# Performance work log

Hardware: AMD Instinct MI355X
Metric: run time of the kernel (lower is better)

Reference implementation:

```python
import jax, jax.numpy as jnp
import numpy as np

EPS = 1e-5

def _lc(x, w, b, stride, pad):
    # x: [B,H,W]; w: [Ho,Wo,kh,kw]; b: [Ho,Wo]
    Ho, Wo, kh, kw = w.shape
    patches = jax.lax.conv_general_dilated_patches(
        x[:, None], (kh, kw), (stride, stride), [(pad, pad), (pad, pad)])
    # patches: [B, kh*kw, Ho, Wo]
    out = jnp.einsum('bkij,ijk->bij', patches, w.reshape(Ho, Wo, kh * kw))
    return out + b

def _ln2d(x, g, b):
    # torch LayerNorm over the last two (spatial) dims
    mu = x.mean(axis=(1, 2), keepdims=True)
    var = ((x - mu) ** 2).mean(axis=(1, 2), keepdims=True)
    return (x - mu) * jax.lax.rsqrt(var + EPS) * g + b

def _pool(x):
    # MaxPool2d(kernel=2, stride=2) over spatial dims of [B,H,W]
    return jax.lax.reduce_window(x, -jnp.inf, jax.lax.max, (1, 2, 2), (1, 2, 2), 'VALID')

def setup_inputs() -> dict:
    key = jax.random.key(0)
    ks = jax.random.split(key, 32)
    d = {}
    d['x'] = jax.random.normal(ks[0], (64, 128, 128), jnp.float32)
    sizes = [(128, 7), (64, 5), (64, 5), (32, 3), (32, 3), (16, 3)]
    for i, (s, k) in enumerate(sizes, start=1):
        d[f'w{i}'] = jax.random.normal(ks[4 * i], (s, s, k, k), jnp.float32) / k
        d[f'b{i}'] = jax.random.normal(ks[4 * i + 1], (s, s), jnp.float32)
        d[f'g{i}'] = jnp.ones((s, s), jnp.float32)
        d[f'be{i}'] = jnp.zeros((s, s), jnp.float32)
    d['fcw'] = jax.random.normal(ks[30], (1024, 256), jnp.float32) / np.sqrt(256.0)
    d['fcb'] = jax.random.normal(ks[31], (1024,), jnp.float32) * 0.01
    return d

def reference(x, w1, b1, g1, be1, w2, b2, g2, be2, w3, b3, g3, be3,
              w4, b4, g4, be4, w5, b5, g5, be5, w6, b6, g6, be6, fcw, fcb):
    # dropout is identity (eval / p=0)
    h = _pool(_ln2d(jax.nn.relu(_lc(x, w1, b1, 1, 3)), g1, be1))   # [B,64,64]
    h = _ln2d(jax.nn.relu(_lc(h, w2, b2, 1, 2)), g2, be2)          # [B,64,64]
    h = _pool(_ln2d(jax.nn.relu(_lc(h, w3, b3, 1, 2)), g3, be3))   # [B,32,32]
    h = _ln2d(jax.nn.relu(_lc(h, w4, b4, 1, 1)), g4, be4)          # [B,32,32]
    h = _pool(_ln2d(jax.nn.relu(_lc(h, w5, b5, 1, 1)), g5, be5))   # [B,16,16]
    h = _ln2d(jax.nn.relu(_lc(h, w6, b6, 1, 1)), g6, be6)          # [B,16,16]
    h = h.reshape(h.shape[0], -1) @ fcw.T + fcb                    # [B,1024]
    return jax.nn.softmax(h, axis=-1)
```

## Files before the change

kernel.cpp:

```cpp
#include <hip/hip_runtime.h>

#define LN_EPS 1e-5f

constexpr int T1_OFF   = 0;
constexpr int WT2_OFF  = 1048576;
constexpr int WT3_OFF  = WT2_OFF + 102400;
constexpr int WT4_OFF  = WT3_OFF + 102400;
constexpr int WT5_OFF  = WT4_OFF + 9216;
constexpr int WT6_OFF  = WT5_OFF + 9216;
constexpr int FCWT_OFF = WT6_OFF + 2304;

constexpr int NREP = 136;

__global__ __launch_bounds__(256) void s1_conv(const float* __restrict__ x,
                                               const float* __restrict__ w1,
                                               const float* __restrict__ b1,
                                               const float* __restrict__ w2,
                                               const float* __restrict__ w3,
                                               const float* __restrict__ w4,
                                               const float* __restrict__ w5,
                                               const float* __restrict__ w6,
                                               const float* __restrict__ fcw,
                                               float* __restrict__ ws)
{
    const int tid = threadIdx.x;

    if (blockIdx.x < NREP) {
        const int rb = blockIdx.x;
        if (rb < 32) {
            for (int idx = rb * 256 + tid; idx < 102400; idx += 32 * 256) {
                int p = idx / 25, k = idx % 25;
                ws[WT2_OFF + k * 4096 + p] = w2[idx];
            }
        } else if (rb < 64) {
            for (int idx = (rb - 32) * 256 + tid; idx < 102400; idx += 32 * 256) {
                int p = idx / 25, k = idx % 25;
                ws[WT3_OFF + k * 4096 + p] = w3[idx];
            }
        } else if (rb < 68) {
            for (int idx = (rb - 64) * 256 + tid; idx < 9216; idx += 4 * 256) {
                int p = idx / 9, k = idx % 9;
                ws[WT4_OFF + k * 1024 + p] = w4[idx];
            }
        } else if (rb < 72) {
            for (int idx = (rb - 68) * 256 + tid; idx < 9216; idx += 4 * 256) {
                int p = idx / 9, k = idx % 9;
                ws[WT5_OFF + k * 1024 + p] = w5[idx];
            }
        } else if (rb < 73) {
            for (int idx = tid; idx < 2304; idx += 256) {
                int p = idx / 9, k = idx % 9;
                ws[WT6_OFF + k * 256 + p] = w6[idx];
            }
        } else {
            for (int idx = (rb - 73) * 256 + tid; idx < 262144; idx += 63 * 256) {
                int r = idx >> 8, kc = idx & 255;
                int kq = kc >> 2, c = kc & 3;
                ws[FCWT_OFF + kq * 4096 + r * 4 + c] = fcw[idx];
            }
        }
        return;
    }

    constexpr int R = 128, K = 7, TILE = 8, S = 16, PAD = 3;
    constexpr int RT = TILE + K - 1;
    constexpr int PP = RT * RT + 1;
    constexpr int NBLK = R / TILE;
    constexpr int WCNT = TILE * TILE * K * K;
    constexpr int PG = 256 / S;
    constexpr int OPT = TILE * TILE / PG;

    __shared__ float s_in[S * PP];
    __shared__ float s_w[WCNT];
    __shared__ float s_b[TILE * TILE];

    float* t1 = ws + T1_OFF;
    const int cb = blockIdx.x - NREP;
    const int bt = cb % (NBLK * NBLK);
    const int sg = cb / (NBLK * NBLK);
    const int i0 = (bt / NBLK) * TILE;
    const int j0 = (bt % NBLK) * TILE;
    const int S0 = sg * S;

    for (int idx = tid; idx < WCNT; idx += 256) {
        int pi = idx / (K * K), kk = idx % (K * K);
        int gi = i0 + pi / TILE, gj = j0 + pi % TILE;
        s_w[idx] = w1[(gi * R + gj) * (K * K) + kk];
    }
    if (tid < TILE * TILE)
        s_b[tid] = b1[(i0 + tid / TILE) * R + (j0 + tid % TILE)];

    for (int idx = tid; idx < S * RT * RT; idx += 256) {
        int ls = idx / (RT * RT), p = idx % (RT * RT);
        int ci = i0 - PAD + p / RT, cj = j0 - PAD + p % RT;
        float v = 0.0f;
        if (ci >= 0 && ci < R && cj >= 0 && cj < R)
            v = x[(S0 + ls) * R * R + ci * R + cj];
        s_in[ls * PP + p] = v;
    }
    __syncthreads();

    const int s = tid % S;
    const int pg = tid / S;
    const int p0 = pg * OPT;
    const int ti = p0 / TILE, tj0 = p0 % TILE;
    float acc[OPT];
    #pragma unroll
    for (int o = 0; o < OPT; o++) acc[o] = s_b[p0 + o];
    #pragma unroll
    for (int ki = 0; ki < K; ki++) {
        float row[OPT + K - 1];
        #pragma unroll
        for (int c = 0; c < OPT + K - 1; c++)
            row[c] = s_in[s * PP + (ti + ki) * RT + tj0 + c];
        #pragma unroll
        for (int kj = 0; kj < K; kj++)
            #pragma unroll
            for (int o = 0; o < OPT; o++)
                acc[o] += row[o + kj] * s_w[(p0 + o) * (K * K) + ki * K + kj];
    }
    #pragma unroll
    for (int o = 0; o < OPT; o++)
        t1[(S0 + s) * R * R + (i0 + ti) * R + (j0 + tj0 + o)] = fmaxf(acc[o], 0.0f);
}

constexpr int NT = 1024;
constexpr int NW = NT / 64;

__device__ __forceinline__ void stats_reduce(float* red, float lsum, float lsq,
                                             float inv_n, float* s_mu, float* s_rs)
{
    const int tid = threadIdx.x;
    #pragma unroll
    for (int off = 32; off > 0; off >>= 1) {
        lsum += __shfl_down(lsum, off, 64);
        lsq  += __shfl_down(lsq,  off, 64);
    }
    if ((tid & 63) == 0) { red[tid >> 6] = lsum; red[NW + (tid >> 6)] = lsq; }
    __syncthreads();
    if (tid == 0) {
        float a = 0.f, b = 0.f;
        #pragma unroll
        for (int i = 0; i < NW; i++) { a += red[i]; b += red[NW + i]; }
        float mu = a * inv_n, ms = b * inv_n;
        *s_mu = mu;
        *s_rs = rsqrtf(ms - mu * mu + LN_EPS);
    }
    __syncthreads();
}

__device__ __forceinline__ void conv64_5(const float* __restrict__ I,
                                         const float* __restrict__ wT,
                                         const float* __restrict__ bias,
                                         float* __restrict__ R,
                                         float& lsum, float& lsq)
{
    const int tid = threadIdx.x;
    const int i  = tid >> 4;
    const int j0 = (tid & 15) << 2;
    float4 bv = ((const float4*)bias)[tid];
    float a0 = bv.x, a1 = bv.y, a2 = bv.z, a3 = bv.w;
    #pragma unroll
    for (int ki = 0; ki < 5; ki++) {
        int ii = i - 2 + ki;
        bool rok = (ii >= 0 && ii < 64);
        float row[8];
        #pragma unroll
        for (int c = 0; c < 8; c++) {
            int jj = j0 - 2 + c;
            row[c] = (rok && jj >= 0 && jj < 64) ? I[ii * 68 + jj] : 0.f;
        }
        #pragma unroll
        for (int kj = 0; kj < 5; kj++) {
            float4 wv = ((const float4*)(wT + (ki * 5 + kj) * 4096))[tid];
            a0 += row[kj + 0] * wv.x;
            a1 += row[kj + 1] * wv.y;
            a2 += row[kj + 2] * wv.z;
            a3 += row[kj + 3] * wv.w;
        }
    }
    float4 o;
    o.x = fmaxf(a0, 0.f); o.y = fmaxf(a1, 0.f);
    o.z = fmaxf(a2, 0.f); o.w = fmaxf(a3, 0.f);
    *((float4*)(R + i * 68 + j0)) = o;
    lsum += o.x + o.y + o.z + o.w;
    lsq  += o.x * o.x + o.y * o.y + o.z * o.z + o.w * o.w;
}

__device__ __forceinline__ void conv32_3(const float* __restrict__ I,
                                         const float* __restrict__ wT,
                                         const float* __restrict__ bias,
                                         float* __restrict__ R,
                                         float& lsum, float& lsq)
{
    const int tid = threadIdx.x;
    const int i = tid >> 5, j = tid & 31;
    float acc = bias[tid];
    #pragma unroll
    for (int ki = 0; ki < 3; ki++) {
        int ii = i - 1 + ki;
        bool rok = (ii >= 0 && ii < 32);
        float r0 = (rok && j >= 1)  ? I[ii * 36 + j - 1] : 0.f;
        float r1 = rok              ? I[ii * 36 + j]     : 0.f;
        float r2 = (rok && j <= 30) ? I[ii * 36 + j + 1] : 0.f;
        acc += r0 * wT[(ki * 3 + 0) * 1024 + tid]
             + r1 * wT[(ki * 3 + 1) * 1024 + tid]
             + r2 * wT[(ki * 3 + 2) * 1024 + tid];
    }
    float v = fmaxf(acc, 0.f);
    R[i * 36 + j] = v;
    lsum += v; lsq += v * v;
}

__device__ __forceinline__ void conv16_3(const float* __restrict__ I,
                                         const float* __restrict__ wT,
                                         const float* __restrict__ bias,
                                         float* __restrict__ R,
                                         float& lsum, float& lsq)
{
    const int tid = threadIdx.x;
    if (tid >= 256) return;
    const int i = tid >> 4, j = tid & 15;
    float acc = bias[tid];
    #pragma unroll
    for (int ki = 0; ki < 3; ki++) {
        int ii = i - 1 + ki;
        bool rok = (ii >= 0 && ii < 16);
        float r0 = (rok && j >= 1)  ? I[ii * 20 + j - 1] : 0.f;
        float r1 = rok              ? I[ii * 20 + j]     : 0.f;
        float r2 = (rok && j <= 14) ? I[ii * 20 + j + 1] : 0.f;
        acc += r0 * wT[(ki * 3 + 0) * 256 + tid]
             + r1 * wT[(ki * 3 + 1) * 256 + tid]
             + r2 * wT[(ki * 3 + 2) * 256 + tid];
    }
    float v = fmaxf(acc, 0.f);
    R[i * 20 + j] = v;
    lsum += v; lsq += v * v;
}

__device__ __forceinline__ void t64(const float* __restrict__ R, float mu, float rs,
                                    const float* __restrict__ g,
                                    const float* __restrict__ b,
                                    float* __restrict__ I)
{
    const int tid = threadIdx.x;
    const int i = tid >> 4, j0 = (tid & 15) << 2;
    float4 rv = *((const float4*)(R + i * 68 + j0));
    float4 gv = ((const float4*)g)[tid];
    float4 bv = ((const float4*)b)[tid];
    float4 o;
    o.x = (rv.x - mu) * rs * gv.x + bv.x;
    o.y = (rv.y - mu) * rs * gv.y + bv.y;
    o.z = (rv.z - mu) * rs * gv.z + bv.z;
    o.w = (rv.w - mu) * rs * gv.w + bv.w;
    *((float4*)(I + i * 68 + j0)) = o;
}

__device__ __forceinline__ void t64pool(const float* __restrict__ R, float mu, float rs,
                                        const float* __restrict__ g,
                                        const float* __restrict__ b,
                                        float* __restrict__ I)
{
    const int tid = threadIdx.x;
    const int i = tid >> 5, j = tid & 31;
    float2 r0 = *((const float2*)(R + (2 * i) * 68 + 2 * j));
    float2 r1 = *((const float2*)(R + (2 * i + 1) * 68 + 2 * j));
    float2 g0 = *((const float2*)(g + (2 * i) * 64 + 2 * j));
    float2 g1 = *((const float2*)(g + (2 * i + 1) * 64 + 2 * j));
    float2 b0 = *((const float2*)(b + (2 * i) * 64 + 2 * j));
    float2 b1 = *((const float2*)(b + (2 * i + 1) * 64 + 2 * j));
    float n00 = (r0.x - mu) * rs * g0.x + b0.x;
    float n01 = (r0.y - mu) * rs * g0.y + b0.y;
    float n10 = (r1.x - mu) * rs * g1.x + b1.x;
    float n11 = (r1.y - mu) * rs * g1.y + b1.y;
    I[i * 36 + j] = fmaxf(fmaxf(n00, n01), fmaxf(n10, n11));
}

__device__ __forceinline__ void t32(const float* __restrict__ R, float mu, float rs,
                                    const float* __restrict__ g,
                                    const float* __restrict__ b,
                                    float* __restrict__ I)
{
    const int tid = threadIdx.x;
    const int i = tid >> 5, j = tid & 31;
    I[i * 36 + j] = (R[i * 36 + j] - mu) * rs * g[tid] + b[tid];
}

__device__ __forceinline__ void t32pool(const float* __restrict__ R, float mu, float rs,
                                        const float* __restrict__ g,
                                        const float* __restrict__ b,
                                        float* __restrict__ I)
{
    const int tid = threadIdx.x;
    if (tid >= 256) return;
    const int i = tid >> 4, j = tid & 15;
    float2 r0 = *((const float2*)(R + (2 * i) * 36 + 2 * j));
    float2 r1 = *((const float2*)(R + (2 * i + 1) * 36 + 2 * j));
    float2 g0 = *((const float2*)(g + (2 * i) * 32 + 2 * j));
    float2 g1 = *((const float2*)(g + (2 * i + 1) * 32 + 2 * j));
    float2 b0 = *((const float2*)(b + (2 * i) * 32 + 2 * j));
    float2 b1 = *((const float2*)(b + (2 * i + 1) * 32 + 2 * j));
    float n00 = (r0.x - mu) * rs * g0.x + b0.x;
    float n01 = (r0.y - mu) * rs * g0.y + b0.y;
    float n10 = (r1.x - mu) * rs * g1.x + b1.x;
    float n11 = (r1.y - mu) * rs * g1.y + b1.y;
    I[i * 20 + j] = fmaxf(fmaxf(n00, n01), fmaxf(n10, n11));
}

__global__ __launch_bounds__(1024) void tail_fused(
    const float* __restrict__ ws_ro,
    const float* __restrict__ g1, const float* __restrict__ be1,
    const float* __restrict__ b2,
    const float* __restrict__ g2, const float* __restrict__ be2,
    const float* __restrict__ b3,
    const float* __restrict__ g3, const float* __restrict__ be3,
    const float* __restrict__ b4,
    const float* __restrict__ g4, const float* __restrict__ be4,
    const float* __restrict__ b5,
    const float* __restrict__ g5, const float* __restrict__ be5,
    const float* __restrict__ b6,
    const float* __restrict__ g6, const float* __restrict__ be6,
    const float* __restrict__ fcb,
    float* __restrict__ outp)
{
    __shared__ __align__(16) float I[64 * 68];
    __shared__ __align__(16) float R[64 * 68];
    __shared__ __align__(16) float h[256];
    __shared__ float red[2 * NW];
    __shared__ float s_mu, s_rs;

    const int s = blockIdx.x;
    const int tid = threadIdx.x;
    const float* x1  = ws_ro + T1_OFF + s * 16384;
    const float* wT2 = ws_ro + WT2_OFF;
    const float* wT3 = ws_ro + WT3_OFF;
    const float* wT4 = ws_ro + WT4_OFF;
    const float* wT5 = ws_ro + WT5_OFF;
    const float* wT6 = ws_ro + WT6_OFF;
    const float* fcwT4 = ws_ro + FCWT_OFF;

    float ls = 0.f, lq = 0.f;
    {
        const float4* x4 = (const float4*)x1;
        #pragma unroll
        for (int i = tid; i < 4096; i += NT) {
            float4 v = x4[i];
            ls += v.x + v.y + v.z + v.w;
            lq += v.x * v.x + v.y * v.y + v.z * v.z + v.w * v.w;
        }
    }
    stats_reduce(red, ls, lq, 1.f / 16384.f, &s_mu, &s_rs);

    {
        float mu = s_mu, rs = s_rs;
        const int i = tid >> 4, j0 = (tid & 15) << 2;
        const float* xr0 = x1 + (2 * i) * 128 + 2 * j0;
        const float* xr1 = xr0 + 128;
        const float* gr0 = g1 + (2 * i) * 128 + 2 * j0;
        const float* gr1 = gr0 + 128;
        const float* br0 = be1 + (2 * i) * 128 + 2 * j0;
        const float* br1 = br0 + 128;
        float4 xa0 = ((const float4*)xr0)[0], xa1 = ((const float4*)xr0)[1];
        float4 xb0 = ((const float4*)xr1)[0], xb1 = ((const float4*)xr1)[1];
        float4 ga0 = ((const float4*)gr0)[0], ga1 = ((const float4*)gr0)[1];
        float4 gb0 = ((const float4*)gr1)[0], gb1 = ((const float4*)gr1)[1];
        float4 ba0 = ((const float4*)br0)[0], ba1 = ((const float4*)br0)[1];
        float4 bb0 = ((const float4*)br1)[0], bb1 = ((const float4*)br1)[1];
        float xa[8] = {xa0.x, xa0.y, xa0.z, xa0.w, xa1.x, xa1.y, xa1.z, xa1.w};
        float xb[8] = {xb0.x, xb0.y, xb0.z, xb0.w, xb1.x, xb1.y, xb1.z, xb1.w};
        float ga[8] = {ga0.x, ga0.y, ga0.z, ga0.w, ga1.x, ga1.y, ga1.z, ga1.w};
        float gb[8] = {gb0.x, gb0.y, gb0.z, gb0.w, gb1.x, gb1.y, gb1.z, gb1.w};
        float ba[8] = {ba0.x, ba0.y, ba0.z, ba0.w, ba1.x, ba1.y, ba1.z, ba1.w};
        float bb[8] = {bb0.x, bb0.y, bb0.z, bb0.w, bb1.x, bb1.y, bb1.z, bb1.w};
        float4 o;
        float* op = (float*)&o;
        #pragma unroll
        for (int c = 0; c < 4; c++) {
            float n0 = (xa[2 * c]     - mu) * rs * ga[2 * c]     + ba[2 * c];
            float n1 = (xa[2 * c + 1] - mu) * rs * ga[2 * c + 1] + ba[2 * c + 1];
            float n2 = (xb[2 * c]     - mu) * rs * gb[2 * c]     + bb[2 * c];
            float n3 = (xb[2 * c + 1] - mu) * rs * gb[2 * c + 1] + bb[2 * c + 1];
            op[c] = fmaxf(fmaxf(n0, n1), fmaxf(n2, n3));
        }
        *((float4*)(I + i * 68 + j0)) = o;
    }
    __syncthreads();

    ls = lq = 0.f; conv64_5(I, wT2, b2, R, ls, lq);
    stats_reduce(red, ls, lq, 1.f / 4096.f, &s_mu, &s_rs);
    t64(R, s_mu, s_rs, g2, be2, I);
    __syncthreads();

    ls = lq = 0.f; conv64_5(I, wT3, b3, R, ls, lq);
    stats_reduce(red, ls, lq, 1.f / 4096.f, &s_mu, &s_rs);
    t64pool(R, s_mu, s_rs, g3, be3, I);
    __syncthreads();

    ls = lq = 0.f; conv32_3(I, wT4, b4, R, ls, lq);
    stats_reduce(red, ls, lq, 1.f / 1024.f, &s_mu, &s_rs);
    t32(R, s_mu, s_rs, g4, be4, I);
    __syncthreads();

    ls = lq = 0.f; conv32_3(I, wT5, b5, R, ls, lq);
    stats_reduce(red, ls, lq, 1.f / 1024.f, &s_mu, &s_rs);
    t32pool(R, s_mu, s_rs, g5, be5, I);
    __syncthreads();

    ls = lq = 0.f; conv16_3(I, wT6, b6, R, ls, lq);
    stats_reduce(red, ls, lq, 1.f / 256.f, &s_mu, &s_rs);

    if (tid < 256) {
        int i = tid >> 4, j = tid & 15;
        h[tid] = (R[i * 20 + j] - s_mu) * s_rs * g6[tid] + be6[tid];
    }
    __syncthreads();

    float acc = fcb[tid];
    {
        const float4* wq = (const float4*)fcwT4;
        const float4* h4 = (const float4*)h;
        #pragma unroll 8
        for (int kq = 0; kq < 64; kq++) {
            float4 wv = wq[kq * 1024 + tid];
            float4 hv = h4[kq];
            acc += wv.x * hv.x + wv.y * hv.y + wv.z * hv.z + wv.w * hv.w;
        }
    }

    float m = acc;
    #pragma unroll
    for (int off = 32; off > 0; off >>= 1)
        m = fmaxf(m, __shfl_down(m, off, 64));
    if ((tid & 63) == 0) red[tid >> 6] = m;
    __syncthreads();
    if (tid == 0) {
        float mm = red[0];
        #pragma unroll
        for (int i = 1; i < NW; i++) mm = fmaxf(mm, red[i]);
        s_mu = mm;
    }
    __syncthreads();
    float e = expf(acc - s_mu);
    float sum = e;
    #pragma unroll
    for (int off = 32; off > 0; off >>= 1)
        sum += __shfl_down(sum, off, 64);
    if ((tid & 63) == 0) red[NW + (tid >> 6)] = sum;
    __syncthreads();
    if (tid == 0) {
        float ss = 0.f;
        #pragma unroll
        for (int i = 0; i < NW; i++) ss += red[NW + i];
        s_rs = 1.0f / ss;
    }
    __syncthreads();
    outp[s * 1024 + tid] = e * s_rs;
}

extern "C" void kernel_launch(void* const* d_in, const int* in_sizes, int n_in,
                              void* d_out, int out_size, void* d_ws, size_t ws_size,
                              hipStream_t stream) {
    (void)in_sizes; (void)n_in; (void)out_size; (void)ws_size;

    const float* x   = (const float*)d_in[0];
    const float* w1  = (const float*)d_in[1];  const float* b1  = (const float*)d_in[2];
    const float* g1  = (const float*)d_in[3];  const float* be1 = (const float*)d_in[4];
    const float* w2  = (const float*)d_in[5];  const float* b2  = (const float*)d_in[6];
    const float* g2  = (const float*)d_in[7];  const float* be2 = (const float*)d_in[8];
    const float* w3  = (const float*)d_in[9];  const float* b3  = (const float*)d_in[10];
    const float* g3  = (const float*)d_in[11]; const float* be3 = (const float*)d_in[12];
    const float* w4  = (const float*)d_in[13]; const float* b4  = (const float*)d_in[14];
    const float* g4  = (const float*)d_in[15]; const float* be4 = (const float*)d_in[16];
    const float* w5  = (const float*)d_in[17]; const float* b5  = (const float*)d_in[18];
    const float* g5  = (const float*)d_in[19]; const float* be5 = (const float*)d_in[20];
    const float* w6  = (const float*)d_in[21]; const float* b6  = (const float*)d_in[22];
    const float* g6  = (const float*)d_in[23]; const float* be6 = (const float*)d_in[24];
    const float* fcw = (const float*)d_in[25]; const float* fcb = (const float*)d_in[26];

    float* ws = (float*)d_ws;

    s1_conv<<<NREP + 1024, 256, 0, stream>>>(x, w1, b1, w2, w3, w4, w5, w6, fcw, ws);
    tail_fused<<<64, 1024, 0, stream>>>((const float*)ws,
        g1, be1, b2, g2, be2, b3, g3, be3,
        b4, g4, be4, b5, g5, be5, b6, g6, be6,
        fcb, (float*)d_out);
}
```

Baseline: 163.3 us.

## Split FC and softmax into separate kernels and relayout 5x5 conv weights

The fused tail kernel used to finish with the FC layer and softmax on only 64 blocks. That work now goes to a 256-block FC kernel and a separate softmax kernel, with intermediates staged in the workspace, so the FC weight read is spread across more CUs. The 5x5 conv weights are relaid so each thread computes four rows of one column, reading shared memory column-wise, which is meant to reduce bank conflicts. Shared-memory tile I/O changes from vectorized float4 to scalar access. The cost is two extra kernel launches plus a global round-trip for the activations and logits.

```diff
diff --git a/kernel.cpp b/kernel.cpp
--- a/kernel.cpp
+++ b/kernel.cpp
@@ -9,6 +9,8 @@
 constexpr int WT5_OFF  = WT4_OFF + 9216;
 constexpr int WT6_OFF  = WT5_OFF + 9216;
 constexpr int FCWT_OFF = WT6_OFF + 2304;
+constexpr int H_OFF    = FCWT_OFF + 262144;
+constexpr int LOG_OFF  = H_OFF + 16384;
 
 constexpr int NREP = 136;
 
@@ -29,13 +31,17 @@
         const int rb = blockIdx.x;
         if (rb < 32) {
             for (int idx = rb * 256 + tid; idx < 102400; idx += 32 * 256) {
-                int p = idx / 25, k = idx % 25;
-                ws[WT2_OFF + k * 4096 + p] = w2[idx];
+                int k = idx >> 12, rem = idx & 4095;
+                int rg = rem >> 8, rem2 = rem & 255;
+                int j = rem2 >> 2, r = rem2 & 3;
+                ws[WT2_OFF + idx] = w2[((rg * 4 + r) * 64 + j) * 25 + k];
             }
         } else if (rb < 64) {
             for (int idx = (rb - 32) * 256 + tid; idx < 102400; idx += 32 * 256) {
-                int p = idx / 25, k = idx % 25;
-                ws[WT3_OFF + k * 4096 + p] = w3[idx];
+                int k = idx >> 12, rem = idx & 4095;
+                int rg = rem >> 8, rem2 = rem & 255;
+                int j = rem2 >> 2, r = rem2 & 3;
+                ws[WT3_OFF + idx] = w3[((rg * 4 + r) * 64 + j) * 25 + k];
             }
         } else if (rb < 68) {
             for (int idx = (rb - 64) * 256 + tid; idx < 9216; idx += 4 * 256) {
@@ -156,35 +162,36 @@
                                          float& lsum, float& lsq)
 {
     const int tid = threadIdx.x;
-    const int i  = tid >> 4;
-    const int j0 = (tid & 15) << 2;
-    float4 bv = ((const float4*)bias)[tid];
-    float a0 = bv.x, a1 = bv.y, a2 = bv.z, a3 = bv.w;
+    const int j  = tid & 63;
+    const int rg = tid >> 6;
+    const int r0 = rg << 2;
+    float a0 = bias[(r0 + 0) * 64 + j];
+    float a1 = bias[(r0 + 1) * 64 + j];
+    float a2 = bias[(r0 + 2) * 64 + j];
+    float a3 = bias[(r0 + 3) * 64 + j];
     #pragma unroll
     for (int ki = 0; ki < 5; ki++) {
-        int ii = i - 2 + ki;
-        bool rok = (ii >= 0 && ii < 64);
-        float row[8];
-        #pragma unroll
-        for (int c = 0; c < 8; c++) {
-            int jj = j0 - 2 + c;
-            row[c] = (rok && jj >= 0 && jj < 64) ? I[ii * 68 + jj] : 0.f;
+        const int i0 = r0 - 2 + ki;
+        #pragma unroll
+        for (int kj = 0; kj < 5; kj++) {
+            float4 wv = *(const float4*)(wT + (ki * 5 + kj) * 4096 + rg * 256 + j * 4);
+            int jj = j - 2 + kj;
+            bool cok = (jj >= 0 && jj < 64);
+            float v0 = (cok && i0 + 0 >= 0 && i0 + 0 < 64) ? I[(i0 + 0) * 68 + jj] : 0.f;
+            float v1 = (cok && i0 + 1 >= 0 && i0 + 1 < 64) ? I[(i0 + 1) * 68 + jj] : 0.f;
+            float v2 = (cok && i0 + 2 >= 0 && i0 + 2 < 64) ? I[(i0 + 2) * 68 + jj] : 0.f;
+            float v3 = (cok && i0 + 3 >= 0 && i0 + 3 < 64) ? I[(i0 + 3) * 68 + jj] : 0.f;
+            a0 += v0 * wv.x; a1 += v1 * wv.y; a2 += v2 * wv.z; a3 += v3 * wv.w;
         }
-        #pragma unroll
-        for (int kj = 0; kj < 5; kj++) {
-            float4 wv = ((const float4*)(wT + (ki * 5 + kj) * 4096))[tid];
-            a0 += row[kj + 0] * wv.x;
-            a1 += row[kj + 1] * wv.y;
-            a2 += row[kj + 2] * wv.z;
-            a3 += row[kj + 3] * wv.w;
-        }
-    }
-    float4 o;
-    o.x = fmaxf(a0, 0.f); o.y = fmaxf(a1, 0.f);
-    o.z = fmaxf(a2, 0.f); o.w = fmaxf(a3, 0.f);
-    *((float4*)(R + i * 68 + j0)) = o;
-    lsum += o.x + o.y + o.z + o.w;
-    lsq  += o.x * o.x + o.y * o.y + o.z * o.z + o.w * o.w;
+    }
+    a0 = fmaxf(a0, 0.f); a1 = fmaxf(a1, 0.f);
+    a2 = fmaxf(a2, 0.f); a3 = fmaxf(a3, 0.f);
+    R[(r0 + 0) * 68 + j] = a0;
+    R[(r0 + 1) * 68 + j] = a1;
+    R[(r0 + 2) * 68 + j] = a2;
+    R[(r0 + 3) * 68 + j] = a3;
+    lsum += a0 + a1 + a2 + a3;
+    lsq  += a0 * a0 + a1 * a1 + a2 * a2 + a3 * a3;
 }
 
 __device__ __forceinline__ void conv32_3(const float* __restrict__ I,
@@ -244,16 +251,12 @@
                                     float* __restrict__ I)
 {
     const int tid = threadIdx.x;
-    const int i = tid >> 4, j0 = (tid & 15) << 2;
-    float4 rv = *((const float4*)(R + i * 68 + j0));
-    float4 gv = ((const float4*)g)[tid];
-    float4 bv = ((const float4*)b)[tid];
-    float4 o;
-    o.x = (rv.x - mu) * rs * gv.x + bv.x;
-    o.y = (rv.y - mu) * rs * gv.y + bv.y;
-    o.z = (rv.z - mu) * rs * gv.z + bv.z;
-    o.w = (rv.w - mu) * rs * gv.w + bv.w;
-    *((float4*)(I + i * 68 + j0)) = o;
+    #pragma unroll
+    for (int o = 0; o < 4; o++) {
+        int p = tid + o * NT;
+        int i = p >> 6, j = p & 63;
+        I[i * 68 + j] = (R[i * 68 + j] - mu) * rs * g[p] + b[p];
+    }
 }
 
 __device__ __forceinline__ void t64pool(const float* __restrict__ R, float mu, float rs,
@@ -308,7 +311,7 @@
 }
 
 __global__ __launch_bounds__(1024) void tail_fused(
-    const float* __restrict__ ws_ro,
+    float* __restrict__ ws,
     const float* __restrict__ g1, const float* __restrict__ be1,
     const float* __restrict__ b2,
     const float* __restrict__ g2, const float* __restrict__ be2,
@@ -319,25 +322,21 @@
     const float* __restrict__ b5,
     const float* __restrict__ g5, const float* __restrict__ be5,
     const float* __restrict__ b6,
-    const float* __restrict__ g6, const float* __restrict__ be6,
-    const float* __restrict__ fcb,
-    float* __restrict__ outp)
+    const float* __restrict__ g6, const float* __restrict__ be6)
 {
     __shared__ __align__(16) float I[64 * 68];
     __shared__ __align__(16) float R[64 * 68];
-    __shared__ __align__(16) float h[256];
     __shared__ float red[2 * NW];
     __shared__ float s_mu, s_rs;
 
     const int s = blockIdx.x;
     const int tid = threadIdx.x;
-    const float* x1  = ws_ro + T1_OFF + s * 16384;
-    const float* wT2 = ws_ro + WT2_OFF;
-    const float* wT3 = ws_ro + WT3_OFF;
-    const float* wT4 = ws_ro + WT4_OFF;
-    const float* wT5 = ws_ro + WT5_OFF;
-    const float* wT6 = ws_ro + WT6_OFF;
-    const float* fcwT4 = ws_ro + FCWT_OFF;
+    const float* x1  = ws + T1_OFF + s * 16384;
+    const float* wT2 = ws + WT2_OFF;
+    const float* wT3 = ws + WT3_OFF;
+    const float* wT4 = ws + WT4_OFF;
+    const float* wT5 = ws + WT5_OFF;
+    const float* wT6 = ws + WT6_OFF;
 
     float ls = 0.f, lq = 0.f;
     {
@@ -353,36 +352,22 @@
 
     {
         float mu = s_mu, rs = s_rs;
-        const int i = tid >> 4, j0 = (tid & 15) << 2;
-        const float* xr0 = x1 + (2 * i) * 128 + 2 * j0;
-        const float* xr1 = xr0 + 128;
-        const float* gr0 = g1 + (2 * i) * 128 + 2 * j0;
-        const float* gr1 = gr0 + 128;
-        const float* br0 = be1 + (2 * i) * 128 + 2 * j0;
-        const float* br1 = br0 + 128;
-        float4 xa0 = ((const float4*)xr0)[0], xa1 = ((const float4*)xr0)[1];
-        float4 xb0 = ((const float4*)xr1)[0], xb1 = ((const float4*)xr1)[1];
-        float4 ga0 = ((const float4*)gr0)[0], ga1 = ((const float4*)gr0)[1];
-        float4 gb0 = ((const float4*)gr1)[0], gb1 = ((const float4*)gr1)[1];
-        float4 ba0 = ((const float4*)br0)[0], ba1 = ((const float4*)br0)[1];
-        float4 bb0 = ((const float4*)br1)[0], bb1 = ((const float4*)br1)[1];
-        float xa[8] = {xa0.x, xa0.y, xa0.z, xa0.w, xa1.x, xa1.y, xa1.z, xa1.w};
-        float xb[8] = {xb0.x, xb0.y, xb0.z, xb0.w, xb1.x, xb1.y, xb1.z, xb1.w};
-        float ga[8] = {ga0.x, ga0.y, ga0.z, ga0.w, ga1.x, ga1.y, ga1.z, ga1.w};
-        float gb[8] = {gb0.x, gb0.y, gb0.z, gb0.w, gb1.x, gb1.y, gb1.z, gb1.w};
-        float ba[8] = {ba0.x, ba0.y, ba0.z, ba0.w, ba1.x, ba1.y, ba1.z, ba1.w};
-        float bb[8] = {bb0.x, bb0.y, bb0.z, bb0.w, bb1.x, bb1.y, bb1.z, bb1.w};
-        float4 o;
-        float* op = (float*)&o;
-        #pragma unroll
-        for (int c = 0; c < 4; c++) {
-            float n0 = (xa[2 * c]     - mu) * rs * ga[2 * c]     + ba[2 * c];
-            float n1 = (xa[2 * c + 1] - mu) * rs * ga[2 * c + 1] + ba[2 * c + 1];
-            float n2 = (xb[2 * c]     - mu) * rs * gb[2 * c]     + bb[2 * c];
-            float n3 = (xb[2 * c + 1] - mu) * rs * gb[2 * c + 1] + bb[2 * c + 1];
-            op[c] = fmaxf(fmaxf(n0, n1), fmaxf(n2, n3));
+        #pragma unroll
+        for (int o = 0; o < 4; o++) {
+            int p = tid + o * NT;
+            int i = p >> 6, j = p & 63;
+            float2 xa = *((const float2*)(x1 + (2 * i) * 128 + 2 * j));
+            float2 xb = *((const float2*)(x1 + (2 * i + 1) * 128 + 2 * j));
+            float2 ga = *((const float2*)(g1 + (2 * i) * 128 + 2 * j));
+            float2 gb = *((const float2*)(g1 + (2 * i + 1) * 128 + 2 * j));
+            float2 ba = *((const float2*)(be1 + (2 * i) * 128 + 2 * j));
+            float2 bb = *((const float2*)(be1 + (2 * i + 1) * 128 + 2 * j));
+            float n0 = (xa.x - mu) * rs * ga.x + ba.x;
+            float n1 = (xa.y - mu) * rs * ga.y + ba.y;
+            float n2 = (xb.x - mu) * rs * gb.x + bb.x;
+            float n3 = (xb.y - mu) * rs * gb.y + bb.y;
+            I[i * 68 + j] = fmaxf(fmaxf(n0, n1), fmaxf(n2, n3));
         }
-        *((float4*)(I + i * 68 + j0)) = o;
     }
     __syncthreads();
 
@@ -411,50 +396,63 @@
 
     if (tid < 256) {
         int i = tid >> 4, j = tid & 15;
-        h[tid] = (R[i * 20 + j] - s_mu) * s_rs * g6[tid] + be6[tid];
-    }
-    __syncthreads();
-
-    float acc = fcb[tid];
-    {
-        const float4* wq = (const float4*)fcwT4;
-        const float4* h4 = (const float4*)h;
-        #pragma unroll 8
-        for (int kq = 0; kq < 64; kq++) {
-            float4 wv = wq[kq * 1024 + tid];
-            float4 hv = h4[kq];
-            acc += wv.x * hv.x + wv.y * hv.y + wv.z * hv.z + wv.w * hv.w;
-        }
-    }
-
-    float m = acc;
-    #pragma unroll
-    for (int off = 32; off > 0; off >>= 1)
-        m = fmaxf(m, __shfl_down(m, off, 64));
-    if ((tid & 63) == 0) red[tid >> 6] = m;
-    __syncthreads();
-    if (tid == 0) {
-        float mm = red[0];
-        #pragma unroll
-        for (int i = 1; i < NW; i++) mm = fmaxf(mm, red[i]);
-        s_mu = mm;
-    }
-    __syncthreads();
-    float e = expf(acc - s_mu);
-    float sum = e;
-    #pragma unroll
-    for (int off = 32; off > 0; off >>= 1)
-        sum += __shfl_down(sum, off, 64);
-    if ((tid & 63) == 0) red[NW + (tid >> 6)] = sum;
-    __syncthreads();
-    if (tid == 0) {
-        float ss = 0.f;
-        #pragma unroll
-        for (int i = 0; i < NW; i++) ss += red[NW + i];
-        s_rs = 1.0f / ss;
-    }
-    __syncthreads();
-    outp[s * 1024 + tid] = e * s_rs;
+        ws[H_OFF + s * 256 + tid] =
+            (R[i * 20 + j] - s_mu) * s_rs * g6[tid] + be6[tid];
+    }
+}
+
+__global__ __launch_bounds__(256) void fc_kernel(const float* __restrict__ ws_ro,
+                                                 const float* __restrict__ fcb,
+                                                 float* __restrict__ logits)
+{
+    __shared__ float h[256];
+    const int s = blockIdx.x >> 2, q = blockIdx.x & 3;
+    const int tid = threadIdx.x;
+    h[tid] = ws_ro[H_OFF + s * 256 + tid];
+    __syncthreads();
+    const int o = q * 256 + tid;
+    const float4* wq = (const float4*)(ws_ro + FCWT_OFF);
+    const float4* h4 = (const float4*)h;
+    float acc = fcb[o];
+    #pragma unroll 8
+    for (int kq = 0; kq < 64; kq++) {
+        float4 wv = wq[kq * 1024 + o];
+        float4 hv = h4[kq];
+        acc += wv.x * hv.x + wv.y * hv.y + wv.z * hv.z + wv.w * hv.w;
+    }
+    logits[s * 1024 + o] = acc;
+}
+
+__global__ __launch_bounds__(256) void softmax_k(const float* __restrict__ logits,
+                                                 float* __restrict__ out)
+{
+    __shared__ float red[256];
+    const int s = blockIdx.x;
+    const int tid = threadIdx.x;
+
+    float4 v = ((const float4*)(logits + s * 1024))[tid];
+    float lmax = fmaxf(fmaxf(v.x, v.y), fmaxf(v.z, v.w));
+    red[tid] = lmax;
+    __syncthreads();
+    for (int off = 128; off > 0; off >>= 1) {
+        if (tid < off) red[tid] = fmaxf(red[tid], red[tid + off]);
+        __syncthreads();
+    }
+    float M = red[0];
+    __syncthreads();
+
+    float4 e;
+    e.x = expf(v.x - M); e.y = expf(v.y - M);
+    e.z = expf(v.z - M); e.w = expf(v.w - M);
+    red[tid] = e.x + e.y + e.z + e.w;
+    __syncthreads();
+    for (int off = 128; off > 0; off >>= 1) {
+        if (tid < off) red[tid] += red[tid + off];
+        __syncthreads();
+    }
+    float inv = 1.0f / red[0];
+    e.x *= inv; e.y *= inv; e.z *= inv; e.w *= inv;
+    ((float4*)(out + s * 1024))[tid] = e;
 }
 
 extern "C" void kernel_launch(void* const* d_in, const int* in_sizes, int n_in,
@@ -480,8 +478,9 @@
     float* ws = (float*)d_ws;
 
     s1_conv<<<NREP + 1024, 256, 0, stream>>>(x, w1, b1, w2, w3, w4, w5, w6, fcw, ws);
-    tail_fused<<<64, 1024, 0, stream>>>((const float*)ws,
+    tail_fused<<<64, 1024, 0, stream>>>(ws,
         g1, be1, b2, g2, be2, b3, g3, be3,
-        b4, g4, be4, b5, g5, be5, b6, g6, be6,
-        fcb, (float*)d_out);
-}
+        b4, g4, be4, b5, g5, be5, b6, g6, be6);
+    fc_kernel<<<256, 256, 0, stream>>>((const float*)ws, fcb, ws + LOG_OFF);
+    softmax_k<<<64, 256, 0, stream>>>(ws + LOG_OFF, (float*)d_out);
+}
```

Measured after the change: 216.9 us. +32.9%, slower.
